# Kernel optimization log

Measured on AMD Instinct MI355X. Metric: run time of the kernel, lower is better.

## Reference

```python
import jax, jax.numpy as jnp
import numpy as np


def setup_inputs() -> dict:
    key = jax.random.key(0)
    kx, ks = jax.random.split(key)
    B, N, D = 2048, 65536, 64
    X = jax.random.normal(kx, (B, D), dtype=jnp.float32)
    svs = jax.random.normal(ks, (N, D), dtype=jnp.float32)
    # scale ~ 1 / mean pairwise squared distance; for iid N(0,1) data E[d^2] = 2D
    scale = jnp.asarray(1.0 / (2.0 * D), dtype=jnp.float32)
    return {"X": X, "svs": svs, "scale": scale}


def reference(X, svs, scale):
    N, D = svs.shape
    x2 = jnp.sum(X * X, axis=-1, keepdims=True)            # [B, 1]
    y2 = jnp.sum(svs * svs, axis=-1)                       # [N]
    d2 = x2 + y2[None, :] - 2.0 * jnp.einsum('bd,nd->bn', X, svs)  # [B, N]
    log_p = (jax.scipy.special.logsumexp(-scale * d2, axis=-1)
             - jnp.log(jnp.asarray(N, dtype=X.dtype))
             + (D / 2) * jnp.log(scale / jnp.pi))
    return log_p
```

## Files before the change

### kernel.cpp

```cpp
#include <hip/hip_runtime.h>
#include <hip/hip_bf16.h>

typedef __attribute__((ext_vector_type(8))) short short8;
typedef __attribute__((ext_vector_type(4))) float f32x4;

#define LOG2E 1.4426950408889634f
#define PI_F 3.14159265358979323846f
#define NTOT 65536
#define BTOT 2048
#define DIM 64
#define SPLITS 64
#define NITER 8
#define NTILES 512

#define OFF_SVSBF 0u
#define OFF_XBF   8388608u
#define OFF_B2    8650752u
#define OFF_A2    8912896u
#define OFF_PART  8921088u
#define WS_NEEDED 9445376u

__device__ __forceinline__ unsigned short f2bf(float f) {
    union { __hip_bfloat16 h; unsigned short u; } c;
    c.h = __float2bfloat16(f);
    return c.u;
}

__device__ __forceinline__ int swz(int row, int kbyte) {
    return row * 128 + (kbyte ^ ((row & 7) << 4));
}

__global__ __launch_bounds__(256) void kde_prep(
    const float* __restrict__ X, const float* __restrict__ svs,
    const float* __restrict__ scale_p, unsigned short* __restrict__ svs_bf,
    unsigned short* __restrict__ x_bf, float* __restrict__ b2,
    float* __restrict__ a2nat) {
    const float scale = scale_p[0];
    const int tid = threadIdx.x;
    const int blk = blockIdx.x;
    if (blk < NTILES) {
        for (int i = 0; i < 4; ++i) {
            int g = i * 256 + tid;
            int row = g >> 3, grp = g & 7;
            const float* src = svs + ((size_t)blk * 128 + row) * DIM + grp * 8;
            float4 v0 = *(const float4*)src;
            float4 v1 = *(const float4*)(src + 4);
            float ss = v0.x * v0.x + v0.y * v0.y + v0.z * v0.z + v0.w * v0.w +
                       v1.x * v1.x + v1.y * v1.y + v1.z * v1.z + v1.w * v1.w;
            short8 o;
            o[0] = f2bf(v0.x); o[1] = f2bf(v0.y); o[2] = f2bf(v0.z); o[3] = f2bf(v0.w);
            o[4] = f2bf(v1.x); o[5] = f2bf(v1.y); o[6] = f2bf(v1.z); o[7] = f2bf(v1.w);
            int dgrp = grp ^ (row & 7);
            *(short8*)(svs_bf + (size_t)blk * 8192 + row * 64 + dgrp * 8) = o;
            ss += __shfl_xor(ss, 1, 64);
            ss += __shfl_xor(ss, 2, 64);
            ss += __shfl_xor(ss, 4, 64);
            if (grp == 0) b2[blk * 128 + row] = -scale * LOG2E * ss;
        }
    } else {
        const int t16 = blk - NTILES;
        const float C1 = 2.0f * scale * LOG2E;
        for (int i = 0; i < 4; ++i) {
            int g = i * 256 + tid;
            int row = g >> 3, grp = g & 7;
            const float* src = X + ((size_t)t16 * 128 + row) * DIM + grp * 8;
            float4 v0 = *(const float4*)src;
            float4 v1 = *(const float4*)(src + 4);
            float ss = v0.x * v0.x + v0.y * v0.y + v0.z * v0.z + v0.w * v0.w +
                       v1.x * v1.x + v1.y * v1.y + v1.z * v1.z + v1.w * v1.w;
            short8 o;
            o[0] = f2bf(v0.x * C1); o[1] = f2bf(v0.y * C1);
            o[2] = f2bf(v0.z * C1); o[3] = f2bf(v0.w * C1);
            o[4] = f2bf(v1.x * C1); o[5] = f2bf(v1.y * C1);
            o[6] = f2bf(v1.z * C1); o[7] = f2bf(v1.w * C1);
            *(short8*)(x_bf + ((size_t)t16 * 128 + row) * 64 + grp * 8) = o;
            ss += __shfl_xor(ss, 1, 64);
            ss += __shfl_xor(ss, 2, 64);
            ss += __shfl_xor(ss, 4, 64);
            if (grp == 0) a2nat[t16 * 128 + row] = -scale * ss;
        }
    }
}

__global__ __launch_bounds__(256) void kde_main2(
    const unsigned short* __restrict__ svs_bf,
    const unsigned short* __restrict__ x_bf, const float* __restrict__ b2,
    float* __restrict__ partials) {
    __shared__ __align__(16) unsigned char ldsB[2][16384];
    __shared__ __align__(16) float ldsb2[1024];

    const int tid = threadIdx.x, lane = tid & 63, wave = tid >> 6;
    const int mtile = blockIdx.x, nsplit = blockIdx.y;
    const int rowbase = mtile * 128;
    const int col = lane & 15, krow = lane >> 4;

    short8 afrag[2][2];
    {
        int arow = rowbase + wave * 32 + col;
        for (int mf = 0; mf < 2; ++mf)
            for (int kf = 0; kf < 2; ++kf)
                afrag[mf][kf] = *(const short8*)(x_bf + (size_t)(arow + mf * 16) * 64 +
                                                 krow * 8 + kf * 32);
    }
    asm volatile("s_waitcnt vmcnt(0)" ::: "memory");

    {
        const float* gb2 = b2 + nsplit * 1024 + wave * 256 + lane * 4;
        __builtin_amdgcn_global_load_lds(
            (const __attribute__((address_space(1))) void*)gb2,
            (__attribute__((address_space(3))) void*)&ldsb2[wave * 256], 16, 0, 0);
    }
    const unsigned char* gsv =
        (const unsigned char*)svs_bf + (size_t)nsplit * NITER * 16384;
#define ISSUE_TILE(t_, buf_)                                                      \
    do {                                                                          \
        const unsigned char* gt =                                                 \
            gsv + (size_t)(t_)*16384 + (size_t)wave * 4096 + lane * 16;           \
        for (int ii = 0; ii < 4; ++ii)                                            \
            __builtin_amdgcn_global_load_lds(                                     \
                (const __attribute__((address_space(1))) void*)(gt + ii * 1024),  \
                (__attribute__((address_space(3))) void*)&ldsB[buf_][(wave * 4 + ii) * 1024], \
                16, 0, 0);                                                        \
    } while (0)
    ISSUE_TILE(0, 0);
    ISSUE_TILE(1, 1);

    float s[2][4] = {{0.f, 0.f, 0.f, 0.f}, {0.f, 0.f, 0.f, 0.f}};

#pragma unroll
    for (int it = 0; it < NITER; ++it) {
        if (it < NITER - 1)
            asm volatile("s_waitcnt vmcnt(4)" ::: "memory");
        else
            asm volatile("s_waitcnt vmcnt(0)" ::: "memory");
        asm volatile("s_barrier" ::: "memory");
        const unsigned char* buf = ldsB[it & 1];
#pragma unroll
        for (int nf = 0; nf < 8; ++nf) {
            float b2l = ldsb2[it * 128 + nf * 16 + col];
            int brow = nf * 16 + col;
            int kb = krow * 16;
            short8 bb0 = *(const short8*)(buf + swz(brow, kb));
            short8 bb1 = *(const short8*)(buf + swz(brow, kb + 64));
#pragma unroll
            for (int mf = 0; mf < 2; ++mf) {
                f32x4 acc = {b2l, b2l, b2l, b2l};
                acc = __builtin_amdgcn_mfma_f32_16x16x32_bf16(afrag[mf][0], bb0,
                                                              acc, 0, 0, 0);
                acc = __builtin_amdgcn_mfma_f32_16x16x32_bf16(afrag[mf][1], bb1,
                                                              acc, 0, 0, 0);
                s[mf][0] += __builtin_amdgcn_exp2f(acc[0]);
                s[mf][1] += __builtin_amdgcn_exp2f(acc[1]);
                s[mf][2] += __builtin_amdgcn_exp2f(acc[2]);
                s[mf][3] += __builtin_amdgcn_exp2f(acc[3]);
            }
        }
        asm volatile("s_barrier" ::: "memory");
        if (it + 2 < NITER) ISSUE_TILE(it + 2, it & 1);
    }
#undef ISSUE_TILE

    for (int mask = 1; mask < 16; mask <<= 1)
        for (int mf = 0; mf < 2; ++mf)
            for (int j = 0; j < 4; ++j)
                s[mf][j] += __shfl_xor(s[mf][j], mask, 64);

    if (col == 0) {
        for (int mf = 0; mf < 2; ++mf)
            for (int j = 0; j < 4; ++j) {
                int row = rowbase + wave * 32 + mf * 16 + krow * 4 + j;
                partials[(size_t)nsplit * BTOT + row] = s[mf][j];
            }
    }
}

__global__ void kde_final2(const float* __restrict__ partials,
                           const float* __restrict__ a2nat,
                           const float* __restrict__ scale_p,
                           float* __restrict__ out) {
    int b = blockIdx.x * 256 + threadIdx.x;
    if (b >= BTOT) return;
    float total = 0.f;
    for (int sidx = 0; sidx < SPLITS; ++sidx)
        total += partials[(size_t)sidx * BTOT + b];
    out[b] = logf(total) + a2nat[b] - logf((float)NTOT) +
             32.0f * logf(scale_p[0] / PI_F);
}

__global__ void fb_rownorm(const float* __restrict__ in,
                           const float* __restrict__ scale_p,
                           float* __restrict__ out, int nrows) {
    int t = blockIdx.x * 256 + threadIdx.x;
    int row = t >> 4;
    if (row >= nrows) return;
    int c4 = t & 15;
    float4 v = *(const float4*)&in[(size_t)row * 64 + c4 * 4];
    float ss = v.x * v.x + v.y * v.y + v.z * v.z + v.w * v.w;
    ss += __shfl_xor(ss, 1, 64);
    ss += __shfl_xor(ss, 2, 64);
    ss += __shfl_xor(ss, 4, 64);
    ss += __shfl_xor(ss, 8, 64);
    if (c4 == 0) out[row] = -scale_p[0] * LOG2E * ss;
}

__global__ __launch_bounds__(256) void fb_main(
    const float* __restrict__ X, const float* __restrict__ svs,
    const float* __restrict__ scale_p, const float* __restrict__ a2,
    const float* __restrict__ b2, float* __restrict__ partials) {
    __shared__ __align__(16) unsigned char ldsA[128 * 128];
    __shared__ __align__(16) unsigned char ldsBf[128 * 128];
    const int tid = threadIdx.x, lane = tid & 63, wave = tid >> 6;
    const int rowbase = blockIdx.x * 128, nbase = blockIdx.y * 512;
    const float C1 = 2.0f * scale_p[0] * LOG2E;
    {
        int r16 = tid >> 4, c4 = tid & 15;
        for (int p = 0; p < 8; ++p) {
            int row = p * 16 + r16;
            float4 v = *(const float4*)&X[(size_t)(rowbase + row) * 64 + c4 * 4];
            uint2 pk;
            pk.x = (unsigned)f2bf(v.x) | ((unsigned)f2bf(v.y) << 16);
            pk.y = (unsigned)f2bf(v.z) | ((unsigned)f2bf(v.w) << 16);
            *(uint2*)(ldsA + swz(row, c4 * 8)) = pk;
        }
    }
    __syncthreads();
    short8 afrag[2][2];
    {
        int arow = wave * 32 + (lane & 15);
        int kb = (lane >> 4) * 16;
        for (int mf = 0; mf < 2; ++mf)
            for (int kf = 0; kf < 2; ++kf)
                afrag[mf][kf] = *(const short8*)(ldsA + swz(arow + mf * 16, kb + kf * 64));
    }
    float a2l[2][4];
    for (int mf = 0; mf < 2; ++mf)
        for (int j = 0; j < 4; ++j)
            a2l[mf][j] = a2[rowbase + wave * 32 + mf * 16 + (lane >> 4) * 4 + j];
    float s[2][4] = {{0.f, 0.f, 0.f, 0.f}, {0.f, 0.f, 0.f, 0.f}};
    for (int itq = 0; itq < 4; ++itq) {
        int nb0 = nbase + itq * 128;
        __syncthreads();
        {
            int r16 = tid >> 4, c4 = tid & 15;
            for (int p = 0; p < 8; ++p) {
                int row = p * 16 + r16;
                float4 v = *(const float4*)&svs[(size_t)(nb0 + row) * 64 + c4 * 4];
                uint2 pk;
                pk.x = (unsigned)f2bf(v.x) | ((unsigned)f2bf(v.y) << 16);
                pk.y = (unsigned)f2bf(v.z) | ((unsigned)f2bf(v.w) << 16);
                *(uint2*)(ldsBf + swz(row, c4 * 8)) = pk;
            }
        }
        float b2l[8];
        for (int nf = 0; nf < 8; ++nf)
            b2l[nf] = b2[nb0 + nf * 16 + (lane & 15)];
        __syncthreads();
        for (int nf = 0; nf < 8; ++nf) {
            int brow = nf * 16 + (lane & 15);
            int kb = (lane >> 4) * 16;
            short8 b0 = *(const short8*)(ldsBf + swz(brow, kb));
            short8 b1 = *(const short8*)(ldsBf + swz(brow, kb + 64));
            for (int mf = 0; mf < 2; ++mf) {
                f32x4 acc = {0.f, 0.f, 0.f, 0.f};
                acc = __builtin_amdgcn_mfma_f32_16x16x32_bf16(afrag[mf][0], b0, acc, 0, 0, 0);
                acc = __builtin_amdgcn_mfma_f32_16x16x32_bf16(afrag[mf][1], b1, acc, 0, 0, 0);
                for (int j = 0; j < 4; ++j) {
                    float e = __builtin_fmaf(C1, acc[j], a2l[mf][j]) + b2l[nf];
                    s[mf][j] += __builtin_amdgcn_exp2f(e);
                }
            }
        }
    }
    for (int mask = 1; mask < 16; mask <<= 1)
        for (int mf = 0; mf < 2; ++mf)
            for (int j = 0; j < 4; ++j)
                s[mf][j] += __shfl_xor(s[mf][j], mask, 64);
    if ((lane & 15) == 0) {
        for (int mf = 0; mf < 2; ++mf)
            for (int j = 0; j < 4; ++j) {
                int row = rowbase + wave * 32 + mf * 16 + (lane >> 4) * 4 + j;
                partials[(size_t)blockIdx.y * BTOT + row] = s[mf][j];
            }
    }
}

__global__ void fb_final(const float* __restrict__ partials,
                         const float* __restrict__ scale_p,
                         float* __restrict__ out) {
    int b = blockIdx.x * 256 + threadIdx.x;
    if (b >= BTOT) return;
    float total = 0.f;
    for (int sidx = 0; sidx < 128; ++sidx)
        total += partials[(size_t)sidx * BTOT + b];
    out[b] = logf(total) - logf((float)NTOT) + 32.0f * logf(scale_p[0] / PI_F);
}

extern "C" void kernel_launch(void* const* d_in, const int* in_sizes, int n_in,
                              void* d_out, int out_size, void* d_ws,
                              size_t ws_size, hipStream_t stream) {
    const float* X = (const float*)d_in[0];
    const float* svs = (const float*)d_in[1];
    const float* scale_p = (const float*)d_in[2];
    unsigned char* ws = (unsigned char*)d_ws;

    if (ws_size >= WS_NEEDED) {
        unsigned short* svs_bf = (unsigned short*)(ws + OFF_SVSBF);
        unsigned short* x_bf = (unsigned short*)(ws + OFF_XBF);
        float* b2 = (float*)(ws + OFF_B2);
        float* a2nat = (float*)(ws + OFF_A2);
        float* partials = (float*)(ws + OFF_PART);
        kde_prep<<<NTILES + 16, 256, 0, stream>>>(X, svs, scale_p, svs_bf, x_bf,
                                                  b2, a2nat);
        dim3 grid(BTOT / 128, SPLITS);
        kde_main2<<<grid, 256, 0, stream>>>(svs_bf, x_bf, b2, partials);
        kde_final2<<<BTOT / 256, 256, 0, stream>>>(partials, a2nat, scale_p,
                                                   (float*)d_out);
    } else {
        float* wsf = (float*)d_ws;
        float* b2 = wsf;
        float* a2 = wsf + NTOT;
        float* partials = wsf + NTOT + BTOT;
        fb_rownorm<<<(NTOT * 16) / 256, 256, 0, stream>>>(svs, scale_p, b2, NTOT);
        fb_rownorm<<<(BTOT * 16) / 256, 256, 0, stream>>>(X, scale_p, a2, BTOT);
        dim3 grid(BTOT / 128, 128);
        fb_main<<<grid, 256, 0, stream>>>(X, svs, scale_p, a2, b2, partials);
        fb_final<<<BTOT / 256, 256, 0, stream>>>(partials, scale_p, (float*)d_out);
    }
}
```

Before: 44.60 us.

## Use 2x2 wave tiling, precomputed exp of column norms, XCD-aware block mapping

Splits the 128x128 block tile among waves as 2x2 (64x64 per wave) instead of 4x1, so each wave loads fewer B fragments from LDS per MFMA. The column-norm term becomes a precomputed exp2 factor applied by FMA after the exp, which lets the accumulator start from zero. Blocks are remapped over a 1D grid so that blocks sharing the same svs split land on the same XCD. Partials double to 128 per row, and a launch-bounds occupancy hint is added. The exp2 of the column norm could underflow for large norms, and the factored product may lose precision.

```diff
diff --git a/kernel.cpp b/kernel.cpp
--- a/kernel.cpp
+++ b/kernel.cpp
@@ -15,10 +15,10 @@
 
 #define OFF_SVSBF 0u
 #define OFF_XBF   8388608u
-#define OFF_B2    8650752u
+#define OFF_EB2   8650752u
 #define OFF_A2    8912896u
 #define OFF_PART  8921088u
-#define WS_NEEDED 9445376u
+#define WS_NEEDED 9969664u
 
 __device__ __forceinline__ unsigned short f2bf(float f) {
     union { __hip_bfloat16 h; unsigned short u; } c;
@@ -33,7 +33,7 @@
 __global__ __launch_bounds__(256) void kde_prep(
     const float* __restrict__ X, const float* __restrict__ svs,
     const float* __restrict__ scale_p, unsigned short* __restrict__ svs_bf,
-    unsigned short* __restrict__ x_bf, float* __restrict__ b2,
+    unsigned short* __restrict__ x_bf, float* __restrict__ eb2,
     float* __restrict__ a2nat) {
     const float scale = scale_p[0];
     const int tid = threadIdx.x;
@@ -55,7 +55,8 @@
             ss += __shfl_xor(ss, 1, 64);
             ss += __shfl_xor(ss, 2, 64);
             ss += __shfl_xor(ss, 4, 64);
-            if (grp == 0) b2[blk * 128 + row] = -scale * LOG2E * ss;
+            if (grp == 0)
+                eb2[blk * 128 + row] = __builtin_amdgcn_exp2f(-scale * LOG2E * ss);
         }
     } else {
         const int t16 = blk - NTILES;
@@ -82,33 +83,36 @@
     }
 }
 
-__global__ __launch_bounds__(256) void kde_main2(
+__global__ __launch_bounds__(256, 4) void kde_main3(
     const unsigned short* __restrict__ svs_bf,
-    const unsigned short* __restrict__ x_bf, const float* __restrict__ b2,
+    const unsigned short* __restrict__ x_bf, const float* __restrict__ eb2,
     float* __restrict__ partials) {
     __shared__ __align__(16) unsigned char ldsB[2][16384];
-    __shared__ __align__(16) float ldsb2[1024];
+    __shared__ __align__(16) float ldseb2[1024];
 
     const int tid = threadIdx.x, lane = tid & 63, wave = tid >> 6;
-    const int mtile = blockIdx.x, nsplit = blockIdx.y;
+    const int bid = blockIdx.x;
+    const int xcd = bid & 7, j = bid >> 3;
+    const int nsplit = ((j & 7) << 3) | xcd;
+    const int mtile = j >> 3;
     const int rowbase = mtile * 128;
+    const int wm = wave >> 1, wn = wave & 1;
     const int col = lane & 15, krow = lane >> 4;
 
-    short8 afrag[2][2];
+    short8 afrag[4][2];
+    for (int mf = 0; mf < 4; ++mf) {
+        int arow = rowbase + wm * 64 + mf * 16 + col;
+        for (int kf = 0; kf < 2; ++kf)
+            afrag[mf][kf] =
+                *(const short8*)(x_bf + (size_t)arow * 64 + krow * 8 + kf * 32);
+    }
+    asm volatile("s_waitcnt vmcnt(0)" ::: "memory");
+
     {
-        int arow = rowbase + wave * 32 + col;
-        for (int mf = 0; mf < 2; ++mf)
-            for (int kf = 0; kf < 2; ++kf)
-                afrag[mf][kf] = *(const short8*)(x_bf + (size_t)(arow + mf * 16) * 64 +
-                                                 krow * 8 + kf * 32);
-    }
-    asm volatile("s_waitcnt vmcnt(0)" ::: "memory");
-
-    {
-        const float* gb2 = b2 + nsplit * 1024 + wave * 256 + lane * 4;
+        const float* gb = eb2 + nsplit * 1024 + wave * 256 + lane * 4;
         __builtin_amdgcn_global_load_lds(
-            (const __attribute__((address_space(1))) void*)gb2,
-            (__attribute__((address_space(3))) void*)&ldsb2[wave * 256], 16, 0, 0);
+            (const __attribute__((address_space(1))) void*)gb,
+            (__attribute__((address_space(3))) void*)&ldseb2[wave * 256], 16, 0, 0);
     }
     const unsigned char* gsv =
         (const unsigned char*)svs_bf + (size_t)nsplit * NITER * 16384;
@@ -125,7 +129,10 @@
     ISSUE_TILE(0, 0);
     ISSUE_TILE(1, 1);
 
-    float s[2][4] = {{0.f, 0.f, 0.f, 0.f}, {0.f, 0.f, 0.f, 0.f}};
+    const f32x4 zacc = {0.f, 0.f, 0.f, 0.f};
+    float s[4][4];
+    for (int mf = 0; mf < 4; ++mf)
+        for (int q = 0; q < 4; ++q) s[mf][q] = 0.f;
 
 #pragma unroll
     for (int it = 0; it < NITER; ++it) {
@@ -136,23 +143,22 @@
         asm volatile("s_barrier" ::: "memory");
         const unsigned char* buf = ldsB[it & 1];
 #pragma unroll
-        for (int nf = 0; nf < 8; ++nf) {
-            float b2l = ldsb2[it * 128 + nf * 16 + col];
-            int brow = nf * 16 + col;
+        for (int nf = 0; nf < 4; ++nf) {
+            int brow = wn * 64 + nf * 16 + col;
             int kb = krow * 16;
             short8 bb0 = *(const short8*)(buf + swz(brow, kb));
             short8 bb1 = *(const short8*)(buf + swz(brow, kb + 64));
+            float eb2l = ldseb2[it * 128 + wn * 64 + nf * 16 + col];
 #pragma unroll
-            for (int mf = 0; mf < 2; ++mf) {
-                f32x4 acc = {b2l, b2l, b2l, b2l};
-                acc = __builtin_amdgcn_mfma_f32_16x16x32_bf16(afrag[mf][0], bb0,
-                                                              acc, 0, 0, 0);
+            for (int mf = 0; mf < 4; ++mf) {
+                f32x4 acc = __builtin_amdgcn_mfma_f32_16x16x32_bf16(
+                    afrag[mf][0], bb0, zacc, 0, 0, 0);
                 acc = __builtin_amdgcn_mfma_f32_16x16x32_bf16(afrag[mf][1], bb1,
                                                               acc, 0, 0, 0);
-                s[mf][0] += __builtin_amdgcn_exp2f(acc[0]);
-                s[mf][1] += __builtin_amdgcn_exp2f(acc[1]);
-                s[mf][2] += __builtin_amdgcn_exp2f(acc[2]);
-                s[mf][3] += __builtin_amdgcn_exp2f(acc[3]);
+                s[mf][0] = __builtin_fmaf(__builtin_amdgcn_exp2f(acc[0]), eb2l, s[mf][0]);
+                s[mf][1] = __builtin_fmaf(__builtin_amdgcn_exp2f(acc[1]), eb2l, s[mf][1]);
+                s[mf][2] = __builtin_fmaf(__builtin_amdgcn_exp2f(acc[2]), eb2l, s[mf][2]);
+                s[mf][3] = __builtin_fmaf(__builtin_amdgcn_exp2f(acc[3]), eb2l, s[mf][3]);
             }
         }
         asm volatile("s_barrier" ::: "memory");
@@ -161,27 +167,27 @@
 #undef ISSUE_TILE
 
     for (int mask = 1; mask < 16; mask <<= 1)
-        for (int mf = 0; mf < 2; ++mf)
-            for (int j = 0; j < 4; ++j)
-                s[mf][j] += __shfl_xor(s[mf][j], mask, 64);
+        for (int mf = 0; mf < 4; ++mf)
+            for (int q = 0; q < 4; ++q)
+                s[mf][q] += __shfl_xor(s[mf][q], mask, 64);
 
     if (col == 0) {
-        for (int mf = 0; mf < 2; ++mf)
-            for (int j = 0; j < 4; ++j) {
-                int row = rowbase + wave * 32 + mf * 16 + krow * 4 + j;
-                partials[(size_t)nsplit * BTOT + row] = s[mf][j];
-            }
-    }
-}
-
-__global__ void kde_final2(const float* __restrict__ partials,
+        for (int mf = 0; mf < 4; ++mf)
+            for (int q = 0; q < 4; ++q) {
+                int row = rowbase + wm * 64 + mf * 16 + krow * 4 + q;
+                partials[(size_t)(nsplit * 2 + wn) * BTOT + row] = s[mf][q];
+            }
+    }
+}
+
+__global__ void kde_final3(const float* __restrict__ partials,
                            const float* __restrict__ a2nat,
                            const float* __restrict__ scale_p,
                            float* __restrict__ out) {
     int b = blockIdx.x * 256 + threadIdx.x;
     if (b >= BTOT) return;
     float total = 0.f;
-    for (int sidx = 0; sidx < SPLITS; ++sidx)
+    for (int sidx = 0; sidx < SPLITS * 2; ++sidx)
         total += partials[(size_t)sidx * BTOT + b];
     out[b] = logf(total) + a2nat[b] - logf((float)NTOT) +
              32.0f * logf(scale_p[0] / PI_F);
@@ -234,8 +240,8 @@
     }
     float a2l[2][4];
     for (int mf = 0; mf < 2; ++mf)
-        for (int j = 0; j < 4; ++j)
-            a2l[mf][j] = a2[rowbase + wave * 32 + mf * 16 + (lane >> 4) * 4 + j];
+        for (int q = 0; q < 4; ++q)
+            a2l[mf][q] = a2[rowbase + wave * 32 + mf * 16 + (lane >> 4) * 4 + q];
     float s[2][4] = {{0.f, 0.f, 0.f, 0.f}, {0.f, 0.f, 0.f, 0.f}};
     for (int itq = 0; itq < 4; ++itq) {
         int nb0 = nbase + itq * 128;
@@ -264,22 +270,22 @@
                 f32x4 acc = {0.f, 0.f, 0.f, 0.f};
                 acc = __builtin_amdgcn_mfma_f32_16x16x32_bf16(afrag[mf][0], b0, acc, 0, 0, 0);
                 acc = __builtin_amdgcn_mfma_f32_16x16x32_bf16(afrag[mf][1], b1, acc, 0, 0, 0);
-                for (int j = 0; j < 4; ++j) {
-                    float e = __builtin_fmaf(C1, acc[j], a2l[mf][j]) + b2l[nf];
-                    s[mf][j] += __builtin_amdgcn_exp2f(e);
+                for (int q = 0; q < 4; ++q) {
+                    float e = __builtin_fmaf(C1, acc[q], a2l[mf][q]) + b2l[nf];
+                    s[mf][q] += __builtin_amdgcn_exp2f(e);
                 }
             }
         }
     }
     for (int mask = 1; mask < 16; mask <<= 1)
         for (int mf = 0; mf < 2; ++mf)
-            for (int j = 0; j < 4; ++j)
-                s[mf][j] += __shfl_xor(s[mf][j], mask, 64);
+            for (int q = 0; q < 4; ++q)
+                s[mf][q] += __shfl_xor(s[mf][q], mask, 64);
     if ((lane & 15) == 0) {
         for (int mf = 0; mf < 2; ++mf)
-            for (int j = 0; j < 4; ++j) {
-                int row = rowbase + wave * 32 + mf * 16 + (lane >> 4) * 4 + j;
-                partials[(size_t)blockIdx.y * BTOT + row] = s[mf][j];
+            for (int q = 0; q < 4; ++q) {
+                int row = rowbase + wave * 32 + mf * 16 + (lane >> 4) * 4 + q;
+                partials[(size_t)blockIdx.y * BTOT + row] = s[mf][q];
             }
     }
 }
@@ -306,14 +312,14 @@
     if (ws_size >= WS_NEEDED) {
         unsigned short* svs_bf = (unsigned short*)(ws + OFF_SVSBF);
         unsigned short* x_bf = (unsigned short*)(ws + OFF_XBF);
-        float* b2 = (float*)(ws + OFF_B2);
+        float* eb2 = (float*)(ws + OFF_EB2);
         float* a2nat = (float*)(ws + OFF_A2);
         float* partials = (float*)(ws + OFF_PART);
         kde_prep<<<NTILES + 16, 256, 0, stream>>>(X, svs, scale_p, svs_bf, x_bf,
-                                                  b2, a2nat);
-        dim3 grid(BTOT / 128, SPLITS);
-        kde_main2<<<grid, 256, 0, stream>>>(svs_bf, x_bf, b2, partials);
-        kde_final2<<<BTOT / 256, 256, 0, stream>>>(partials, a2nat, scale_p,
+                                                  eb2, a2nat);
+        kde_main3<<<BTOT / 128 * SPLITS, 256, 0, stream>>>(svs_bf, x_bf, eb2,
+                                                           partials);
+        kde_final3<<<BTOT / 256, 256, 0, stream>>>(partials, a2nat, scale_p,
                                                    (float*)d_out);
     } else {
         float* wsf = (float*)d_ws;
```

After: 123.2 us. +176.2%, slower.
